# Performance work log

Measured on AMD Instinct MI355X. Metric: run time of the kernel, lower is better.

Reference implementation:

```python
import jax, jax.numpy as jnp
import numpy as np

NEG = -1000000.0  # mask fill value used by the torch module


def setup_inputs() -> dict:
    key = jax.random.key(0)
    k1, k2, k3, k4 = jax.random.split(key, 4)
    B, L, D = 64, 1024, 64
    return {
        "queries": jax.random.normal(k1, (B, L, D), dtype=jnp.float32),
        "keys": jax.random.normal(k2, (B, L, D), dtype=jnp.float32),
        "values": jax.random.normal(k3, (B, L, D), dtype=jnp.float32),
        "valid_lens": jax.random.randint(k4, (B,), 1, 1024, dtype=jnp.int32),
    }


def reference(queries, keys, values, valid_lens):
    d = queries.shape[-1]
    # [B, Lq, Lk] attention scores
    scores = jnp.einsum("bqd,bkd->bqk", queries, keys) / jnp.sqrt(jnp.asarray(d, queries.dtype))
    Lk = scores.shape[-1]
    # sequence mask: key positions >= valid_len are filled with NEG (per batch)
    col = jnp.arange(Lk)  # [Lk]
    mask = col[None, None, :] >= valid_lens[:, None, None]  # [B, 1, Lk] -> broadcasts over q
    scores = jnp.where(mask, NEG, scores)
    attn = jax.nn.softmax(scores, axis=-1)
    # dropout p=0.0 (eval) -> identity
    return jnp.einsum("bqk,bkd->bqd", attn, values)
```

## Files before the change

kernel.cpp:

```cpp
#include <hip/hip_runtime.h>
#include <math.h>


typedef __attribute__((ext_vector_type(4))) float f32x4;
typedef __attribute__((ext_vector_type(8))) short bf16x8;
typedef __attribute__((ext_vector_type(8))) unsigned short u16x8;

constexpr int Bn = 64, Ln = 1024, Dn = 64;
constexpr int NITEM = Bn * 16;
constexpr int NBLK = 768;
constexpr float QSCALE = 0.125f * 1.44269504088896340736f;
constexpr float DEFER_THR = 10.0f;

__device__ inline unsigned short f2bf(float x) {
    unsigned int u = __float_as_uint(x);
    return (unsigned short)((u + 0x7fffu + ((u >> 16) & 1u)) >> 16);
}

__global__ __launch_bounds__(64) void setup_queue(const int* __restrict__ VL,
                                                  int* __restrict__ ws)
{
    const int l = threadIdx.x;
    const int vme = VL[l];
    int rank = 0;
    for (int i = 0; i < 64; ++i) {
        const int vi = __shfl(vme, i, 64);
        rank += (vi > vme) || (vi == vme && i < l);
    }
    ws[1 + rank] = l;
    if (l == 0) ws[0] = NBLK;
}

__global__ __launch_bounds__(256) void flash_attn(
    const float* __restrict__ Q, const float* __restrict__ K,
    const float* __restrict__ V, const int* __restrict__ VL,
    float* __restrict__ O, int* __restrict__ ws)
{
    __shared__ unsigned short kls[2][64 * 64];
    __shared__ unsigned short vls[2][64 * 64];
    __shared__ unsigned short plds[4][16 * 64];

    const int tid = threadIdx.x;
    const int w = tid >> 6, l = tid & 63;
    const int lg = l >> 4, ln = l & 15;

    const int* ord = ws + 1;
    int* ctr = ws;

    const int kr = tid >> 2, kc = (tid & 3) * 16;
    const int sr = ((kr & 0xC) << 2) | ((kr >> 2) & 0xC) | (kr & 3);
    const int vd = l, vk0 = w * 16;

    char* const kls0 = reinterpret_cast<char*>(kls[0]);
    char* const kls1 = reinterpret_cast<char*>(kls[1]);
    char* const vls0 = reinterpret_cast<char*>(vls[0]);
    char* const vls1 = reinterpret_cast<char*>(vls[1]);
    char* const pwb  = reinterpret_cast<char*>(plds[w]);

    const int kb = sr * 128 + kc * 2, ksw = (sr & 7) << 4;
    const int vb = vd * 128 + vk0 * 2, vsw = (vd & 7) << 4;
    const int psw = (ln & 7) << 4;

    f32x4 kpre[4];
    float vpre[16];

    auto stage_write = [&](int pbuf) {
        char* kd = pbuf ? kls1 : kls0;
        char* vdst = pbuf ? vls1 : vls0;
        u16x8 c0, c1;
        #pragma unroll
        for (int j = 0; j < 4; ++j) {
            c0[j]     = f2bf(kpre[0][j]);  c0[j + 4] = f2bf(kpre[1][j]);
            c1[j]     = f2bf(kpre[2][j]);  c1[j + 4] = f2bf(kpre[3][j]);
        }
        *reinterpret_cast<u16x8*>(kd + ((kb)      ^ ksw)) = c0;
        *reinterpret_cast<u16x8*>(kd + ((kb + 16) ^ ksw)) = c1;
        u16x8 v0, v1;
        #pragma unroll
        for (int j = 0; j < 8; ++j) { v0[j] = f2bf(vpre[j]); v1[j] = f2bf(vpre[j + 8]); }
        *reinterpret_cast<u16x8*>(vdst + ((vb)      ^ vsw)) = v0;
        *reinterpret_cast<u16x8*>(vdst + ((vb + 16) ^ vsw)) = v1;
    };

    int item = blockIdx.x;

    while (true) {
        const int b = ord[item >> 4];
        const int qt = item & 15;
        const int qbase = qt * 64 + w * 16;
        const int valid = VL[b];
        const int nkt = (valid + 63) >> 6;

        const float* Kbase = K + (size_t)b * Ln * Dn;
        const float* Vbase = V + (size_t)b * Ln * Dn;

        bf16x8 bq0, bq1;
        {
            const f32x4* qp = reinterpret_cast<const f32x4*>(Q + ((size_t)b * Ln + qbase + ln) * Dn);
            f32x4 q0 = qp[lg * 2], q1 = qp[lg * 2 + 1], q2 = qp[8 + lg * 2], q3 = qp[8 + lg * 2 + 1];
            #pragma unroll
            for (int j = 0; j < 4; ++j) {
                bq0[j]     = (short)f2bf(q0[j] * QSCALE);
                bq0[j + 4] = (short)f2bf(q1[j] * QSCALE);
                bq1[j]     = (short)f2bf(q2[j] * QSCALE);
                bq1[j + 4] = (short)f2bf(q3[j] * QSCALE);
            }
        }

        {
            const f32x4* kp = reinterpret_cast<const f32x4*>(Kbase + (size_t)kr * Dn + kc);
            #pragma unroll
            for (int i = 0; i < 4; ++i) kpre[i] = kp[i];
            const float* vp = Vbase + (size_t)vk0 * Dn + vd;
            #pragma unroll
            for (int i = 0; i < 16; ++i) vpre[i] = vp[(size_t)i * Dn];
        }
        stage_write(0);
        __syncthreads();

        f32x4 acc[4] = {{0.f,0.f,0.f,0.f},{0.f,0.f,0.f,0.f},{0.f,0.f,0.f,0.f},{0.f,0.f,0.f,0.f}};
        float mrow = -1e30f;
        float lrow = 0.f;

        int p = 0;
        for (int kt = 0; kt < nkt; ++kt, p ^= 1) {
            const bool has_next = (kt + 1 < nkt);
            char* kcur = p ? kls1 : kls0;
            char* vcur = p ? vls1 : vls0;

            if (has_next) {
                const f32x4* kp = reinterpret_cast<const f32x4*>(Kbase + (size_t)((kt + 1) * 64 + kr) * Dn + kc);
                #pragma unroll
                for (int i = 0; i < 4; ++i) kpre[i] = kp[i];
                const float* vp = Vbase + (size_t)((kt + 1) * 64 + vk0) * Dn + vd;
                #pragma unroll
                for (int i = 0; i < 16; ++i) vpre[i] = vp[(size_t)i * Dn];
            }

            f32x4 st[4] = {{0.f,0.f,0.f,0.f},{0.f,0.f,0.f,0.f},{0.f,0.f,0.f,0.f},{0.f,0.f,0.f,0.f}};
            #pragma unroll
            for (int t = 0; t < 4; ++t) {
                const int rr = 16 * t + ln, rsw = (rr & 7) << 4;
                bf16x8 ak0 = *reinterpret_cast<const bf16x8*>(kcur + ((rr * 128 + lg * 16)      ^ rsw));
                st[t] = __builtin_amdgcn_mfma_f32_16x16x32_bf16(ak0, bq0, st[t], 0, 0, 0);
                bf16x8 ak1 = *reinterpret_cast<const bf16x8*>(kcur + ((rr * 128 + lg * 16 + 64) ^ rsw));
                st[t] = __builtin_amdgcn_mfma_f32_16x16x32_bf16(ak1, bq1, st[t], 0, 0, 0);
            }

            if (kt * 64 + 64 > valid) {
                #pragma unroll
                for (int t = 0; t < 4; ++t)
                    #pragma unroll
                    for (int j = 0; j < 4; ++j)
                        if (kt * 64 + 16 * lg + 4 * t + j >= valid) st[t][j] = -1e30f;
            }

            float mx;
            {
                float a0 = fmaxf(fmaxf(st[0][0], st[0][1]), fmaxf(st[0][2], st[0][3]));
                float a1 = fmaxf(fmaxf(st[1][0], st[1][1]), fmaxf(st[1][2], st[1][3]));
                float a2 = fmaxf(fmaxf(st[2][0], st[2][1]), fmaxf(st[2][2], st[2][3]));
                float a3 = fmaxf(fmaxf(st[3][0], st[3][1]), fmaxf(st[3][2], st[3][3]));
                mx = fmaxf(fmaxf(a0, a1), fmaxf(a2, a3));
                mx = fmaxf(mx, __shfl_xor(mx, 16, 64));
                mx = fmaxf(mx, __shfl_xor(mx, 32, 64));
            }

            if (__any(mx - mrow > DEFER_THR)) {
                const float mn = fmaxf(mrow, mx);
                const float rs = exp2f(mrow - mn);
                mrow = mn;
                lrow *= rs;
                #pragma unroll
                for (int j = 0; j < 4; ++j) {
                    const float rsj = __shfl(rs, lg * 4 + j, 64);
                    #pragma unroll
                    for (int t = 0; t < 4; ++t) acc[t][j] *= rsj;
                }
            }

            float rsum = 0.f;
            u16x8 plo, phi;
            #pragma unroll
            for (int t = 0; t < 2; ++t)
                #pragma unroll
                for (int j = 0; j < 4; ++j) {
                    const float pv = exp2f(st[t][j] - mrow);
                    rsum += pv;
                    plo[t * 4 + j] = f2bf(pv);
                }
            #pragma unroll
            for (int t = 2; t < 4; ++t)
                #pragma unroll
                for (int j = 0; j < 4; ++j) {
                    const float pv = exp2f(st[t][j] - mrow);
                    rsum += pv;
                    phi[(t - 2) * 4 + j] = f2bf(pv);
                }
            *reinterpret_cast<u16x8*>(pwb + ((ln * 128 + 32 * lg)      ^ psw)) = plo;
            *reinterpret_cast<u16x8*>(pwb + ((ln * 128 + 32 * lg + 16) ^ psw)) = phi;
            rsum += __shfl_xor(rsum, 16, 64);
            rsum += __shfl_xor(rsum, 32, 64);
            lrow += rsum;

            #pragma unroll
            for (int s = 0; s < 2; ++s) {
                bf16x8 pa = *reinterpret_cast<const bf16x8*>(pwb + ((ln * 128 + lg * 16 + 64 * s) ^ psw));
                #pragma unroll
                for (int t = 0; t < 4; ++t) {
                    const int rr = 16 * t + ln, rsw = (rr & 7) << 4;
                    bf16x8 bv = *reinterpret_cast<const bf16x8*>(vcur + ((rr * 128 + lg * 16 + 64 * s) ^ rsw));
                    acc[t] = __builtin_amdgcn_mfma_f32_16x16x32_bf16(pa, bv, acc[t], 0, 0, 0);
                }
            }

            if (has_next) stage_write(p ^ 1);
            __syncthreads();
        }

        const float invl = 1.0f / lrow;
        float inv[4];
        #pragma unroll
        for (int j = 0; j < 4; ++j) inv[j] = __shfl(invl, lg * 4 + j, 64);
        float* Orow = O + ((size_t)b * Ln + qbase) * Dn;
        #pragma unroll
        for (int t = 0; t < 4; ++t) {
            #pragma unroll
            for (int j = 0; j < 4; ++j) {
                const int q = lg * 4 + j;
                const int d = 16 * t + ln;
                Orow[(size_t)q * Dn + d] = acc[t][j] * inv[j];
            }
        }

        if (tid == 0) *reinterpret_cast<int*>(&plds[0][0]) = atomicAdd(ctr, 1);
        __syncthreads();
        item = *reinterpret_cast<const int*>(&plds[0][0]);
        if (item >= NITEM) break;
        __syncthreads();
    }
}

extern "C" void kernel_launch(void* const* d_in, const int* in_sizes, int n_in,
                              void* d_out, int out_size, void* d_ws, size_t ws_size,
                              hipStream_t stream) {
    const float* Q = (const float*)d_in[0];
    const float* K = (const float*)d_in[1];
    const float* V = (const float*)d_in[2];
    const int* VL = (const int*)d_in[3];
    float* O = (float*)d_out;
    int* ws = (int*)d_ws;

    setup_queue<<<1, 64, 0, stream>>>(VL, ws);
    flash_attn<<<NBLK, 256, 0, stream>>>(Q, K, V, VL, O, ws);
}
```

Baseline: 120.7 us.

## Keep P in registers via permuted K layout, use packed bf16 converts

Permutes the K-row order in shared memory so the QK^T MFMA output lanes line up with the A-operand layout of the PV MFMA. The probabilities can then be packed straight from registers instead of round-tripping through a per-wave LDS buffer, and the mask index formula is updated to match. Software bf16 rounding is replaced by the hardware v_cvt_pk_bf16_f32 instruction throughout, and s_setprio raises wave priority around the MFMA blocks. This removes LDS writes/reads and conversion ALU work per tile, at the risk of layout mistakes in the new permutation.

Measured after the change: 117.6 us. 2.6% less time.

```diff
diff --git a/kernel.cpp b/kernel.cpp
--- a/kernel.cpp
+++ b/kernel.cpp
@@ -4,7 +4,7 @@
 
 typedef __attribute__((ext_vector_type(4))) float f32x4;
 typedef __attribute__((ext_vector_type(8))) short bf16x8;
-typedef __attribute__((ext_vector_type(8))) unsigned short u16x8;
+typedef __attribute__((ext_vector_type(4))) unsigned int u32x4;
 
 constexpr int Bn = 64, Ln = 1024, Dn = 64;
 constexpr int NITEM = Bn * 16;
@@ -12,9 +12,10 @@
 constexpr float QSCALE = 0.125f * 1.44269504088896340736f;
 constexpr float DEFER_THR = 10.0f;
 
-__device__ inline unsigned short f2bf(float x) {
-    unsigned int u = __float_as_uint(x);
-    return (unsigned short)((u + 0x7fffu + ((u >> 16) & 1u)) >> 16);
+__device__ inline unsigned int cvt_pk(float lo, float hi) {
+    unsigned int r;
+    asm("v_cvt_pk_bf16_f32 %0, %1, %2" : "=v"(r) : "v"(lo), "v"(hi));
+    return r;
 }
 
 __global__ __launch_bounds__(64) void setup_queue(const int* __restrict__ VL,
@@ -38,7 +39,7 @@
 {
     __shared__ unsigned short kls[2][64 * 64];
     __shared__ unsigned short vls[2][64 * 64];
-    __shared__ unsigned short plds[4][16 * 64];
+    __shared__ int bcast;
 
     const int tid = threadIdx.x;
     const int w = tid >> 6, l = tid & 63;
@@ -48,18 +49,16 @@
     int* ctr = ws;
 
     const int kr = tid >> 2, kc = (tid & 3) * 16;
-    const int sr = ((kr & 0xC) << 2) | ((kr >> 2) & 0xC) | (kr & 3);
+    const int sr = (kr & 0x23) | ((kr & 0x04) << 2) | ((kr & 0x18) >> 1);
     const int vd = l, vk0 = w * 16;
 
     char* const kls0 = reinterpret_cast<char*>(kls[0]);
     char* const kls1 = reinterpret_cast<char*>(kls[1]);
     char* const vls0 = reinterpret_cast<char*>(vls[0]);
     char* const vls1 = reinterpret_cast<char*>(vls[1]);
-    char* const pwb  = reinterpret_cast<char*>(plds[w]);
 
     const int kb = sr * 128 + kc * 2, ksw = (sr & 7) << 4;
     const int vb = vd * 128 + vk0 * 2, vsw = (vd & 7) << 4;
-    const int psw = (ln & 7) << 4;
 
     f32x4 kpre[4];
     float vpre[16];
@@ -67,19 +66,27 @@
     auto stage_write = [&](int pbuf) {
         char* kd = pbuf ? kls1 : kls0;
         char* vdst = pbuf ? vls1 : vls0;
-        u16x8 c0, c1;
-        #pragma unroll
-        for (int j = 0; j < 4; ++j) {
-            c0[j]     = f2bf(kpre[0][j]);  c0[j + 4] = f2bf(kpre[1][j]);
-            c1[j]     = f2bf(kpre[2][j]);  c1[j + 4] = f2bf(kpre[3][j]);
-        }
-        *reinterpret_cast<u16x8*>(kd + ((kb)      ^ ksw)) = c0;
-        *reinterpret_cast<u16x8*>(kd + ((kb + 16) ^ ksw)) = c1;
-        u16x8 v0, v1;
-        #pragma unroll
-        for (int j = 0; j < 8; ++j) { v0[j] = f2bf(vpre[j]); v1[j] = f2bf(vpre[j + 8]); }
-        *reinterpret_cast<u16x8*>(vdst + ((vb)      ^ vsw)) = v0;
-        *reinterpret_cast<u16x8*>(vdst + ((vb + 16) ^ vsw)) = v1;
+        u32x4 c;
+        c[0] = cvt_pk(kpre[0][0], kpre[0][1]);
+        c[1] = cvt_pk(kpre[0][2], kpre[0][3]);
+        c[2] = cvt_pk(kpre[1][0], kpre[1][1]);
+        c[3] = cvt_pk(kpre[1][2], kpre[1][3]);
+        *reinterpret_cast<u32x4*>(kd + ((kb)      ^ ksw)) = c;
+        c[0] = cvt_pk(kpre[2][0], kpre[2][1]);
+        c[1] = cvt_pk(kpre[2][2], kpre[2][3]);
+        c[2] = cvt_pk(kpre[3][0], kpre[3][1]);
+        c[3] = cvt_pk(kpre[3][2], kpre[3][3]);
+        *reinterpret_cast<u32x4*>(kd + ((kb + 16) ^ ksw)) = c;
+        c[0] = cvt_pk(vpre[0],  vpre[1]);
+        c[1] = cvt_pk(vpre[2],  vpre[3]);
+        c[2] = cvt_pk(vpre[4],  vpre[5]);
+        c[3] = cvt_pk(vpre[6],  vpre[7]);
+        *reinterpret_cast<u32x4*>(vdst + ((vb)      ^ vsw)) = c;
+        c[0] = cvt_pk(vpre[8],  vpre[9]);
+        c[1] = cvt_pk(vpre[10], vpre[11]);
+        c[2] = cvt_pk(vpre[12], vpre[13]);
+        c[3] = cvt_pk(vpre[14], vpre[15]);
+        *reinterpret_cast<u32x4*>(vdst + ((vb + 16) ^ vsw)) = c;
     };
 
     int item = blockIdx.x;
@@ -98,13 +105,18 @@
         {
             const f32x4* qp = reinterpret_cast<const f32x4*>(Q + ((size_t)b * Ln + qbase + ln) * Dn);
             f32x4 q0 = qp[lg * 2], q1 = qp[lg * 2 + 1], q2 = qp[8 + lg * 2], q3 = qp[8 + lg * 2 + 1];
-            #pragma unroll
-            for (int j = 0; j < 4; ++j) {
-                bq0[j]     = (short)f2bf(q0[j] * QSCALE);
-                bq0[j + 4] = (short)f2bf(q1[j] * QSCALE);
-                bq1[j]     = (short)f2bf(q2[j] * QSCALE);
-                bq1[j + 4] = (short)f2bf(q3[j] * QSCALE);
-            }
+            u32x4 c;
+            c[0] = cvt_pk(q0[0] * QSCALE, q0[1] * QSCALE);
+            c[1] = cvt_pk(q0[2] * QSCALE, q0[3] * QSCALE);
+            c[2] = cvt_pk(q1[0] * QSCALE, q1[1] * QSCALE);
+            c[3] = cvt_pk(q1[2] * QSCALE, q1[3] * QSCALE);
+            bq0 = reinterpret_cast<bf16x8&>(c);
+            u32x4 d;
+            d[0] = cvt_pk(q2[0] * QSCALE, q2[1] * QSCALE);
+            d[1] = cvt_pk(q2[2] * QSCALE, q2[3] * QSCALE);
+            d[2] = cvt_pk(q3[0] * QSCALE, q3[1] * QSCALE);
+            d[3] = cvt_pk(q3[2] * QSCALE, q3[3] * QSCALE);
+            bq1 = reinterpret_cast<bf16x8&>(d);
         }
 
         {
@@ -138,6 +150,7 @@
             }
 
             f32x4 st[4] = {{0.f,0.f,0.f,0.f},{0.f,0.f,0.f,0.f},{0.f,0.f,0.f,0.f},{0.f,0.f,0.f,0.f}};
+            __builtin_amdgcn_s_setprio(1);
             #pragma unroll
             for (int t = 0; t < 4; ++t) {
                 const int rr = 16 * t + ln, rsw = (rr & 7) << 4;
@@ -146,13 +159,15 @@
                 bf16x8 ak1 = *reinterpret_cast<const bf16x8*>(kcur + ((rr * 128 + lg * 16 + 64) ^ rsw));
                 st[t] = __builtin_amdgcn_mfma_f32_16x16x32_bf16(ak1, bq1, st[t], 0, 0, 0);
             }
+            __builtin_amdgcn_s_setprio(0);
 
             if (kt * 64 + 64 > valid) {
                 #pragma unroll
                 for (int t = 0; t < 4; ++t)
                     #pragma unroll
                     for (int j = 0; j < 4; ++j)
-                        if (kt * 64 + 16 * lg + 4 * t + j >= valid) st[t][j] = -1e30f;
+                        if (kt * 64 + 32 * (t >> 1) + 8 * lg + 4 * (t & 1) + j >= valid)
+                            st[t][j] = -1e30f;
             }
 
             float mx;
@@ -179,40 +194,36 @@
                 }
             }
 
+            float pv[4][4];
             float rsum = 0.f;
-            u16x8 plo, phi;
-            #pragma unroll
-            for (int t = 0; t < 2; ++t)
+            #pragma unroll
+            for (int t = 0; t < 4; ++t)
                 #pragma unroll
                 for (int j = 0; j < 4; ++j) {
-                    const float pv = exp2f(st[t][j] - mrow);
-                    rsum += pv;
-                    plo[t * 4 + j] = f2bf(pv);
+                    pv[t][j] = exp2f(st[t][j] - mrow);
+                    rsum += pv[t][j];
                 }
-            #pragma unroll
-            for (int t = 2; t < 4; ++t)
-                #pragma unroll
-                for (int j = 0; j < 4; ++j) {
-                    const float pv = exp2f(st[t][j] - mrow);
-                    rsum += pv;
-                    phi[(t - 2) * 4 + j] = f2bf(pv);
-                }
-            *reinterpret_cast<u16x8*>(pwb + ((ln * 128 + 32 * lg)      ^ psw)) = plo;
-            *reinterpret_cast<u16x8*>(pwb + ((ln * 128 + 32 * lg + 16) ^ psw)) = phi;
+            u32x4 w0, w1;
+            w0[0] = cvt_pk(pv[0][0], pv[0][1]);  w0[1] = cvt_pk(pv[0][2], pv[0][3]);
+            w0[2] = cvt_pk(pv[1][0], pv[1][1]);  w0[3] = cvt_pk(pv[1][2], pv[1][3]);
+            w1[0] = cvt_pk(pv[2][0], pv[2][1]);  w1[1] = cvt_pk(pv[2][2], pv[2][3]);
+            w1[2] = cvt_pk(pv[3][0], pv[3][1]);  w1[3] = cvt_pk(pv[3][2], pv[3][3]);
+            bf16x8 pa0 = reinterpret_cast<bf16x8&>(w0);
+            bf16x8 pa1 = reinterpret_cast<bf16x8&>(w1);
             rsum += __shfl_xor(rsum, 16, 64);
             rsum += __shfl_xor(rsum, 32, 64);
             lrow += rsum;
 
-            #pragma unroll
-            for (int s = 0; s < 2; ++s) {
-                bf16x8 pa = *reinterpret_cast<const bf16x8*>(pwb + ((ln * 128 + lg * 16 + 64 * s) ^ psw));
-                #pragma unroll
-                for (int t = 0; t < 4; ++t) {
-                    const int rr = 16 * t + ln, rsw = (rr & 7) << 4;
-                    bf16x8 bv = *reinterpret_cast<const bf16x8*>(vcur + ((rr * 128 + lg * 16 + 64 * s) ^ rsw));
-                    acc[t] = __builtin_amdgcn_mfma_f32_16x16x32_bf16(pa, bv, acc[t], 0, 0, 0);
-                }
-            }
+            __builtin_amdgcn_s_setprio(1);
+            #pragma unroll
+            for (int t = 0; t < 4; ++t) {
+                const int rr = 16 * t + ln, rsw = (rr & 7) << 4;
+                bf16x8 bv0 = *reinterpret_cast<const bf16x8*>(vcur + ((rr * 128 + lg * 16)      ^ rsw));
+                acc[t] = __builtin_amdgcn_mfma_f32_16x16x32_bf16(pa0, bv0, acc[t], 0, 0, 0);
+                bf16x8 bv1 = *reinterpret_cast<const bf16x8*>(vcur + ((rr * 128 + lg * 16 + 64) ^ rsw));
+                acc[t] = __builtin_amdgcn_mfma_f32_16x16x32_bf16(pa1, bv1, acc[t], 0, 0, 0);
+            }
+            __builtin_amdgcn_s_setprio(0);
 
             if (has_next) stage_write(p ^ 1);
             __syncthreads();
@@ -233,9 +244,9 @@
             }
         }
 
-        if (tid == 0) *reinterpret_cast<int*>(&plds[0][0]) = atomicAdd(ctr, 1);
+        if (tid == 0) bcast = atomicAdd(ctr, 1);
         __syncthreads();
-        item = *reinterpret_cast<const int*>(&plds[0][0]);
+        item = bcast;
         if (item >= NITEM) break;
         __syncthreads();
     }
```
